# Performance work log

Measured on AMD Instinct MI355X. Metric: run time of the kernel, lower is better.

## Reference

```python
import jax, jax.numpy as jnp
import numpy as np

N, E = 20000, 320000
D_IN, H1, H2, H3, D_OUT = 2048, 512, 128, 32, 2
EPS = 1e-5


def layer_norm(x, g, b):
    mu = jnp.mean(x, axis=-1, keepdims=True)
    var = jnp.mean(jnp.square(x - mu), axis=-1, keepdims=True)
    return (x - mu) * jax.lax.rsqrt(var + EPS) * g + b


def gcn_conv(x, src, dst, n, W, b):
    # x' = D^{-1/2} A_hat D^{-1/2} (x W) + b  (self-loops already in src/dst)
    xw = x @ W
    deg = jax.ops.segment_sum(jnp.ones_like(src, dtype=x.dtype), dst, num_segments=n)
    dinv = jnp.where(deg > 0, jax.lax.rsqrt(jnp.maximum(deg, 1.0)), 0.0)
    norm = dinv[src] * dinv[dst]  # [E+N]
    msg = xw[src] * norm[:, None]
    return jax.ops.segment_sum(msg, dst, num_segments=n) + b


def gat_conv(x, src, dst, n, W, a_src, a_dst, b):
    # single-head GAT, concat=False; PyG defaults: LeakyReLU(0.2), softmax over dst
    xw = x @ W  # [N, H3]
    alpha = jax.nn.leaky_relu(xw[src] @ a_src + xw[dst] @ a_dst, 0.2)  # [E+N]
    amax = jax.ops.segment_max(alpha, dst, num_segments=n)
    e = jnp.exp(alpha - amax[dst])
    denom = jax.ops.segment_sum(e, dst, num_segments=n)
    coef = e / denom[dst]
    out = jax.ops.segment_sum(xw[src] * coef[:, None], dst, num_segments=n)
    return out + b


def setup_inputs() -> dict:
    key = jax.random.key(0)
    ks = jax.random.split(key, 24)
    x = jax.random.normal(ks[0], (N, D_IN), dtype=jnp.float32)
    edge_index = jax.random.randint(ks[1], (2, E), 0, N, dtype=jnp.int64)

    def glorot(k, shape):
        lim = float(np.sqrt(6.0 / (shape[0] + shape[1])))
        return jax.random.uniform(k, shape, jnp.float32, -lim, lim)

    return {
        "x": x, "edge_index": edge_index,
        "W1": glorot(ks[2], (D_IN, H1)), "b1": jnp.zeros((H1,), jnp.float32),
        "ln1_g": jnp.ones((H1,), jnp.float32), "ln1_b": jnp.zeros((H1,), jnp.float32),
        "W2": glorot(ks[3], (H1, H2)), "b2": jnp.zeros((H2,), jnp.float32),
        "ln2_g": jnp.ones((H2,), jnp.float32), "ln2_b": jnp.zeros((H2,), jnp.float32),
        "W3": glorot(ks[4], (H2, H3)), "b3": jnp.zeros((H3,), jnp.float32),
        "ln3_g": jnp.ones((H3,), jnp.float32), "ln3_b": jnp.zeros((H3,), jnp.float32),
        "Wg": glorot(ks[5], (H3, H3)),
        "att_src": jax.random.normal(ks[6], (H3,), jnp.float32) * 0.1,
        "att_dst": jax.random.normal(ks[7], (H3,), jnp.float32) * 0.1,
        "bg": jnp.zeros((H3,), jnp.float32),
        "fc_w": glorot(ks[8], (H3, D_OUT)), "fc_b": jnp.zeros((D_OUT,), jnp.float32),
    }


def reference(x, edge_index, W1, b1, ln1_g, ln1_b, W2, b2, ln2_g, ln2_b,
              W3, b3, ln3_g, ln3_b, Wg, att_src, att_dst, bg, fc_w, fc_b):
    n = x.shape[0]
    loops = jnp.arange(n, dtype=edge_index.dtype)
    src = jnp.concatenate([edge_index[0], loops])
    dst = jnp.concatenate([edge_index[1], loops])

    h = jax.nn.relu(layer_norm(gcn_conv(x, src, dst, n, W1, b1), ln1_g, ln1_b))
    h = jax.nn.relu(layer_norm(gcn_conv(h, src, dst, n, W2, b2), ln2_g, ln2_b))
    h = jax.nn.relu(layer_norm(gcn_conv(h, src, dst, n, W3, b3), ln3_g, ln3_b))
    h = jax.nn.relu(gat_conv(h, src, dst, n, Wg, att_src, att_dst, bg))
    pooled = jnp.mean(h, axis=0, keepdims=True)  # [1, H3]
    return pooled @ fc_w + fc_b  # [1, 2]
```

## Files before the change

kernel.cpp:

```cpp
#include <hip/hip_runtime.h>
#include <hip/hip_bf16.h>
#include <cstdint>
#include <cstddef>

#define N_NODES 20000
#define N_EDGES 320000
#define DIM_IN  2048
#define DIM_H1  512
#define DIM_H2  128
#define DIM_H3  32
#define NPART   64
static constexpr float LN_EPS = 1e-5f;

typedef __bf16 bf16x8 __attribute__((ext_vector_type(8)));
typedef __bf16 bf16x2 __attribute__((ext_vector_type(2)));
typedef float f32x4 __attribute__((ext_vector_type(4)));

__device__ __forceinline__ void glds16(const void* g, void* l) {
  __builtin_amdgcn_global_load_lds(
      (const __attribute__((address_space(1))) unsigned int*)g,
      (__attribute__((address_space(3))) unsigned int*)l, 16, 0, 0);
}

__global__ void detect_fmt_kernel(const void* eraw, int* flag) {
  const int2* p = (const int2*)eraw;
  int all0 = 1;
  for (int i = 0; i < 32; ++i) if (p[i].y != 0) all0 = 0;
  *flag = all0;
}

__global__ void convert_edges_kernel(const void* eraw, const int* __restrict__ flag,
                                     int* __restrict__ src, int* __restrict__ dst, int E) {
  const int is64 = *flag;
  for (int e = blockIdx.x * blockDim.x + threadIdx.x; e < E; e += gridDim.x * blockDim.x) {
    if (is64) {
      const long long* p = (const long long*)eraw;
      src[e] = (int)p[e];
      dst[e] = (int)p[(size_t)E + e];
    } else {
      const int* p = (const int*)eraw;
      src[e] = p[e];
      dst[e] = p[(size_t)E + e];
    }
  }
}

__global__ void count_kernel(const int* __restrict__ dst, int* __restrict__ cnt, int E) {
  for (int e = blockIdx.x * blockDim.x + threadIdx.x; e < E; e += gridDim.x * blockDim.x)
    atomicAdd(&cnt[dst[e]], 1);
}

__global__ __launch_bounds__(1024) void scan_kernel(const int* __restrict__ cnt,
                                                    int* __restrict__ rowptr,
                                                    int* __restrict__ cursor, int n) {
  __shared__ int s[1024];
  const int t = threadIdx.x;
  const int chunk = (n + 1023) / 1024;
  const int beg = t * chunk;
  const int end = min(beg + chunk, n);
  int sum = 0;
  for (int i = beg; i < end; ++i) sum += cnt[i];
  s[t] = sum;
  __syncthreads();
  for (int d = 1; d < 1024; d <<= 1) {
    int v = (t >= d) ? s[t - d] : 0;
    __syncthreads();
    s[t] += v;
    __syncthreads();
  }
  int run = s[t] - sum;
  for (int i = beg; i < end; ++i) { rowptr[i] = run; cursor[i] = run; run += cnt[i]; }
  if (t == 1023) rowptr[n] = s[1023];
}

__global__ void scatter_kernel(const int* __restrict__ src, const int* __restrict__ dst,
                               int* __restrict__ cursor, int* __restrict__ csr_src, int E) {
  for (int e = blockIdx.x * blockDim.x + threadIdx.x; e < E; e += gridDim.x * blockDim.x) {
    int d = dst[e];
    int pos = atomicAdd(&cursor[d], 1);
    csr_src[pos] = src[e];
  }
}

__global__ void dinv_kernel(const int* __restrict__ cnt, float* __restrict__ dinv, int n) {
  int i = blockIdx.x * blockDim.x + threadIdx.x;
  if (i < n) dinv[i] = rsqrtf((float)(cnt[i] + 1));
}

__global__ __launch_bounds__(256) void transpose_cvt_kernel(const float* __restrict__ W,
                                                            __bf16* __restrict__ WT,
                                                            int K, int N) {
  __shared__ float t[32][33];
  const int kb = blockIdx.x * 32, nb = blockIdx.y * 32;
  const int tx = threadIdx.x & 31, ty = threadIdx.x >> 5;
  #pragma unroll
  for (int i = 0; i < 32; i += 8)
    t[ty + i][tx] = W[(size_t)(kb + ty + i) * N + nb + tx];
  __syncthreads();
  #pragma unroll
  for (int i = 0; i < 32; i += 8)
    WT[(size_t)(nb + ty + i) * K + kb + tx] = (__bf16)t[tx][ty + i];
}

template <typename AT, typename CT>
__global__ __launch_bounds__(256) void gemm_glds_kernel(
    const AT* __restrict__ A, const __bf16* __restrict__ BT,
    CT* __restrict__ C, int M, int N, int K) {
  __shared__ __align__(16) AT     Asm[128 * 32];
  __shared__ __align__(16) __bf16 Bsm[128 * 32];
  const int tid = threadIdx.x;
  const int wave = tid >> 6;
  const int lane = tid & 63;
  const int row0 = blockIdx.x * 128;
  const int col0 = blockIdx.y * 128;
  const int wr = (wave >> 1) * 64;
  const int wc = (wave & 1) * 64;

  f32x4 acc[4][4] = {};

  for (int k0 = 0; k0 < K; k0 += 32) {
    if constexpr (sizeof(AT) == 4) {
      #pragma unroll
      for (int i = 0; i < 4; ++i) {
        const int rbase = wave * 32 + i * 8;
        int gr = row0 + rbase + (lane >> 3);
        if (gr >= M) gr = M - 1;
        const int ssrc = (lane & 7) ^ (lane >> 3);
        glds16((const float*)A + (size_t)gr * K + k0 + ssrc * 4, &Asm[rbase * 32]);
      }
    } else {
      #pragma unroll
      for (int i = 0; i < 2; ++i) {
        const int rbase = wave * 32 + i * 16;
        int gr = row0 + rbase + (lane >> 2);
        if (gr >= M) gr = M - 1;
        const int ssrc = (lane & 3) ^ ((lane >> 3) & 3);
        glds16((const __bf16*)A + (size_t)gr * K + k0 + ssrc * 8, &Asm[rbase * 32]);
      }
    }
    #pragma unroll
    for (int j = 0; j < 2; ++j) {
      const int rbase = wave * 32 + j * 16;
      const int gr = col0 + rbase + (lane >> 2);
      const int ssrc = (lane & 3) ^ ((lane >> 3) & 3);
      glds16(BT + (size_t)gr * K + k0 + ssrc * 8, &Bsm[rbase * 32]);
    }
    __syncthreads();

    const int q = lane >> 4;
    bf16x8 af[4], bfr[4];
    #pragma unroll
    for (int m = 0; m < 4; ++m) {
      const int row = wr + m * 16 + (lane & 15);
      if constexpr (sizeof(AT) == 4) {
        const int sw = row & 7;
        f32x4 lo = *(const f32x4*)&((const float*)Asm)[row * 32 + (((2 * q) ^ sw) * 4)];
        f32x4 hi = *(const f32x4*)&((const float*)Asm)[row * 32 + (((2 * q + 1) ^ sw) * 4)];
        bf16x8 o;
        o[0] = (__bf16)lo[0]; o[1] = (__bf16)lo[1]; o[2] = (__bf16)lo[2]; o[3] = (__bf16)lo[3];
        o[4] = (__bf16)hi[0]; o[5] = (__bf16)hi[1]; o[6] = (__bf16)hi[2]; o[7] = (__bf16)hi[3];
        af[m] = o;
      } else {
        const int sw = (row >> 1) & 3;
        af[m] = *(const bf16x8*)&((const __bf16*)Asm)[row * 32 + ((q ^ sw) * 8)];
      }
    }
    #pragma unroll
    for (int n = 0; n < 4; ++n) {
      const int row = wc + n * 16 + (lane & 15);
      const int sw = (row >> 1) & 3;
      bfr[n] = *(const bf16x8*)&Bsm[row * 32 + ((q ^ sw) * 8)];
    }
    #pragma unroll
    for (int m = 0; m < 4; ++m)
      #pragma unroll
      for (int n = 0; n < 4; ++n)
        acc[m][n] = __builtin_amdgcn_mfma_f32_16x16x32_bf16(af[m], bfr[n], acc[m][n], 0, 0, 0);
    __syncthreads();
  }

  #pragma unroll
  for (int m = 0; m < 4; ++m) {
    const int r = row0 + wr + m * 16 + (lane >> 4) * 4;
    #pragma unroll
    for (int n = 0; n < 4; ++n) {
      const int c = col0 + wc + n * 16 + (lane & 15);
      #pragma unroll
      for (int j = 0; j < 4; ++j)
        if (r + j < M) C[(size_t)(r + j) * N + c] = (CT)acc[m][n][j];
    }
  }
}

template <int F, int TPB, typename OutT>
__global__ __launch_bounds__(TPB) void gcn_agg_ln_relu_kernel(
    const float* __restrict__ xw, const float* __restrict__ dinv,
    const int* __restrict__ rowptr, const int* __restrict__ csr_src,
    const float* __restrict__ bias, const float* __restrict__ gamma,
    const float* __restrict__ beta, OutT* __restrict__ h) {
  constexpr int NF = (F + TPB - 1) / TPB;
  const int i = blockIdx.x;
  const int tid = threadIdx.x;
  const float di = dinv[i];
  float acc[NF];
  #pragma unroll
  for (int q = 0; q < NF; ++q) {
    int f = tid + q * TPB;
    acc[q] = (f < F) ? di * xw[(size_t)i * F + f] : 0.f;
  }
  const int beg = rowptr[i], end = rowptr[i + 1];
  for (int j = beg; j < end; ++j) {
    int s = csr_src[j];
    float c = dinv[s];
    const float* row = xw + (size_t)s * F;
    #pragma unroll
    for (int q = 0; q < NF; ++q) {
      int f = tid + q * TPB;
      if (f < F) acc[q] += c * row[f];
    }
  }
  float sum = 0.f, sumsq = 0.f;
  #pragma unroll
  for (int q = 0; q < NF; ++q) {
    int f = tid + q * TPB;
    if (f < F) {
      float v = di * acc[q] + bias[f];
      acc[q] = v;
      sum += v;
      sumsq += v * v;
    }
  }
  #pragma unroll
  for (int m = 32; m >= 1; m >>= 1) {
    sum += __shfl_xor(sum, m);
    sumsq += __shfl_xor(sumsq, m);
  }
  constexpr int NW = TPB / 64;
  __shared__ float red[2][NW];
  const int wid = tid >> 6, lane = tid & 63;
  if (lane == 0) { red[0][wid] = sum; red[1][wid] = sumsq; }
  __syncthreads();
  if (tid == 0) {
    float a = 0.f, b2 = 0.f;
    for (int w = 0; w < NW; ++w) { a += red[0][w]; b2 += red[1][w]; }
    red[0][0] = a;
    red[1][0] = b2;
  }
  __syncthreads();
  const float mu = red[0][0] / F;
  const float var = red[1][0] / F - mu * mu;
  const float rstd = rsqrtf(var + LN_EPS);
  #pragma unroll
  for (int q = 0; q < NF; ++q) {
    int f = tid + q * TPB;
    if (f < F) h[(size_t)i * F + f] = (OutT)fmaxf(0.f, (acc[q] - mu) * rstd * gamma[f] + beta[f]);
  }
}

template <int F, int TPB, typename OutT>
__global__ __launch_bounds__(TPB) void gcn_agg_ln_relu_bf16_kernel(
    const __bf16* __restrict__ xw, const float* __restrict__ dinv,
    const int* __restrict__ rowptr, const int* __restrict__ csr_src,
    const float* __restrict__ bias, const float* __restrict__ gamma,
    const float* __restrict__ beta, OutT* __restrict__ h) {
  static_assert(F == 2 * TPB, "layout");
  const int i = blockIdx.x;
  const int tid = threadIdx.x;
  const int f0 = tid * 2;
  const float di = dinv[i];
  bf16x2 v = *(const bf16x2*)&xw[(size_t)i * F + f0];
  float a0 = di * (float)v[0];
  float a1 = di * (float)v[1];
  const int beg = rowptr[i], end = rowptr[i + 1];
  for (int j = beg; j < end; ++j) {
    int s = csr_src[j];
    float c = dinv[s];
    bf16x2 r = *(const bf16x2*)&xw[(size_t)s * F + f0];
    a0 += c * (float)r[0];
    a1 += c * (float)r[1];
  }
  a0 = di * a0 + bias[f0];
  a1 = di * a1 + bias[f0 + 1];
  float sum = a0 + a1;
  float sumsq = a0 * a0 + a1 * a1;
  #pragma unroll
  for (int m = 32; m >= 1; m >>= 1) {
    sum += __shfl_xor(sum, m);
    sumsq += __shfl_xor(sumsq, m);
  }
  constexpr int NW = TPB / 64;
  __shared__ float red[2][NW];
  const int wid = tid >> 6, lane = tid & 63;
  if (lane == 0) { red[0][wid] = sum; red[1][wid] = sumsq; }
  __syncthreads();
  if (tid == 0) {
    float a = 0.f, b2 = 0.f;
    for (int w = 0; w < NW; ++w) { a += red[0][w]; b2 += red[1][w]; }
    red[0][0] = a;
    red[1][0] = b2;
  }
  __syncthreads();
  const float mu = red[0][0] / F;
  const float var = red[1][0] / F - mu * mu;
  const float rstd = rsqrtf(var + LN_EPS);
  float o0 = fmaxf(0.f, (a0 - mu) * rstd * gamma[f0] + beta[f0]);
  float o1 = fmaxf(0.f, (a1 - mu) * rstd * gamma[f0 + 1] + beta[f0 + 1]);
  if constexpr (sizeof(OutT) == 2) {
    bf16x2 o; o[0] = (__bf16)o0; o[1] = (__bf16)o1;
    *(bf16x2*)&((__bf16*)h)[(size_t)i * F + f0] = o;
  } else {
    float2 o = make_float2(o0, o1);
    *(float2*)&((float*)h)[(size_t)i * F + f0] = o;
  }
}

template <int BM, int BN, int BK, int TM, int TN>
__global__ __launch_bounds__((BM / TM) * (BN / TN)) void sgemm_kernel(
    const float* __restrict__ A, const float* __restrict__ B, float* __restrict__ C,
    int M, int N, int K) {
  constexpr int THREADS = (BM / TM) * (BN / TN);
  __shared__ float As[BK][BM + 4];
  __shared__ float Bs[BK][BN];
  const int tid = threadIdx.x;
  const int tcol = tid % (BN / TN);
  const int trow = tid / (BN / TN);
  const int row0 = blockIdx.y * BM;
  const int col0 = blockIdx.x * BN;
  float acc[TM][TN] = {};
  for (int k0 = 0; k0 < K; k0 += BK) {
    constexpr int A4 = BM * BK / 4;
    #pragma unroll
    for (int i = tid; i < A4; i += THREADS) {
      int r = i / (BK / 4);
      int c4 = i % (BK / 4);
      int gr = row0 + r;
      float4 v = make_float4(0.f, 0.f, 0.f, 0.f);
      if (gr < M) v = *(const float4*)(A + (size_t)gr * K + k0 + c4 * 4);
      As[c4 * 4 + 0][r] = v.x;
      As[c4 * 4 + 1][r] = v.y;
      As[c4 * 4 + 2][r] = v.z;
      As[c4 * 4 + 3][r] = v.w;
    }
    constexpr int B4 = BK * BN / 4;
    #pragma unroll
    for (int i = tid; i < B4; i += THREADS) {
      int r = i / (BN / 4);
      int c4 = i % (BN / 4);
      float4 v = *(const float4*)(B + (size_t)(k0 + r) * N + col0 + c4 * 4);
      *(float4*)(&Bs[r][c4 * 4]) = v;
    }
    __syncthreads();
    #pragma unroll
    for (int kk = 0; kk < BK; ++kk) {
      float ra[TM], rb[TN];
      #pragma unroll
      for (int i = 0; i < TM; ++i) ra[i] = As[kk][trow * TM + i];
      #pragma unroll
      for (int j = 0; j < TN; ++j) rb[j] = Bs[kk][tcol * TN + j];
      #pragma unroll
      for (int i = 0; i < TM; ++i)
        #pragma unroll
        for (int j = 0; j < TN; ++j) acc[i][j] = fmaf(ra[i], rb[j], acc[i][j]);
    }
    __syncthreads();
  }
  #pragma unroll
  for (int i = 0; i < TM; ++i) {
    int gr = row0 + trow * TM + i;
    if (gr >= M) continue;
    #pragma unroll
    for (int j = 0; j < TN; ++j) {
      int gc = col0 + tcol * TN + j;
      if (gc < N) C[(size_t)gr * N + gc] = acc[i][j];
    }
  }
}

__global__ void gat_sdots_kernel(const float* __restrict__ xwg,
                                 const float* __restrict__ att_src,
                                 const float* __restrict__ att_dst,
                                 float* __restrict__ s_src, float* __restrict__ s_dst, int n) {
  int gid = blockIdx.x * blockDim.x + threadIdx.x;
  int node = gid >> 5;
  int l = threadIdx.x & 31;
  if (node >= n) return;
  float v = xwg[(size_t)node * 32 + l];
  float vs = v * att_src[l];
  float vd = v * att_dst[l];
  #pragma unroll
  for (int m = 16; m >= 1; m >>= 1) {
    vs += __shfl_xor(vs, m);
    vd += __shfl_xor(vd, m);
  }
  if (l == 0) { s_src[node] = vs; s_dst[node] = vd; }
}

__device__ __forceinline__ float leaky02(float x) { return x > 0.f ? x : 0.2f * x; }

__global__ __launch_bounds__(64) void gat_agg_kernel(
    const float* __restrict__ xwg, const float* __restrict__ s_src,
    const float* __restrict__ s_dst, const int* __restrict__ rowptr,
    const int* __restrict__ csr_src, const float* __restrict__ bg,
    float* __restrict__ pooled_part) {
  const int i = blockIdx.x;
  const int lane = threadIdx.x;
  const int f = lane & 31;
  const int half = lane >> 5;
  const float sd = s_dst[i];
  float m, den, acc;
  if (half == 0) {
    m = leaky02(s_src[i] + sd);
    den = 1.f;
    acc = xwg[(size_t)i * 32 + f];
  } else {
    m = -3.0e38f;
    den = 0.f;
    acc = 0.f;
  }
  const int beg = rowptr[i], end = rowptr[i + 1];
  for (int j = beg + half; j < end; j += 2) {
    int s = csr_src[j];
    float a = leaky02(s_src[s] + sd);
    float mn = fmaxf(m, a);
    float sc = __expf(m - mn);
    float ea = __expf(a - mn);
    acc = acc * sc + ea * xwg[(size_t)s * 32 + f];
    den = den * sc + ea;
    m = mn;
  }
  float m_o = __shfl_xor(m, 32);
  float den_o = __shfl_xor(den, 32);
  float acc_o = __shfl_xor(acc, 32);
  float mn = fmaxf(m, m_o);
  float sc = __expf(m - mn);
  float so = __expf(m_o - mn);
  float den_t = den * sc + den_o * so;
  float acc_t = acc * sc + acc_o * so;
  float out = fmaxf(acc_t / den_t + bg[f], 0.f);
  if (lane < 32) atomicAdd(&pooled_part[(size_t)(i & (NPART - 1)) * 32 + f], out);
}

__global__ __launch_bounds__(64) void final_fc_kernel(const float* __restrict__ pooled_part,
                                                      const float* __restrict__ fc_w,
                                                      const float* __restrict__ fc_b,
                                                      float* __restrict__ out, float invN) {
  const int lane = threadIdx.x;
  const int f = lane & 31, half = lane >> 5;
  float p = 0.f;
  #pragma unroll
  for (int b = 0; b < NPART / 2; ++b)
    p += pooled_part[(size_t)(half * (NPART / 2) + b) * 32 + f];
  p += __shfl_xor(p, 32);
  p *= invN;
  #pragma unroll
  for (int c = 0; c < 2; ++c) {
    float v = (lane < 32) ? p * fc_w[f * 2 + c] : 0.f;
    #pragma unroll
    for (int m = 16; m >= 1; m >>= 1) v += __shfl_xor(v, m);
    if (lane == 0) out[c] = v + fc_b[c];
  }
}

extern "C" void kernel_launch(void* const* d_in, const int* in_sizes, int n_in,
                              void* d_out, int out_size, void* d_ws, size_t ws_size,
                              hipStream_t stream) {
  const float* x       = (const float*)d_in[0];
  const void*  edges   = d_in[1];
  const float* W1      = (const float*)d_in[2];
  const float* b1      = (const float*)d_in[3];
  const float* ln1_g   = (const float*)d_in[4];
  const float* ln1_b   = (const float*)d_in[5];
  const float* W2      = (const float*)d_in[6];
  const float* b2      = (const float*)d_in[7];
  const float* ln2_g   = (const float*)d_in[8];
  const float* ln2_b   = (const float*)d_in[9];
  const float* W3      = (const float*)d_in[10];
  const float* b3      = (const float*)d_in[11];
  const float* ln3_g   = (const float*)d_in[12];
  const float* ln3_b   = (const float*)d_in[13];
  const float* Wg      = (const float*)d_in[14];
  const float* att_src = (const float*)d_in[15];
  const float* att_dst = (const float*)d_in[16];
  const float* bg      = (const float*)d_in[17];
  const float* fc_w    = (const float*)d_in[18];
  const float* fc_b    = (const float*)d_in[19];
  float* out = (float*)d_out;

  const int N = N_NODES, E = N_EDGES;

  char* ws = (char*)d_ws;
  size_t off = 0;
  auto alloc = [&](size_t bytes) {
    size_t o = off;
    off = (off + bytes + 255) & ~(size_t)255;
    return o;
  };
  size_t o_bufA   = alloc((size_t)N * DIM_H1 * 4);
  size_t o_bufB   = alloc((size_t)N * DIM_H1 * 4);
  size_t o_w1t    = alloc((size_t)DIM_IN * DIM_H1 * 2);
  size_t o_w2t    = alloc((size_t)DIM_H1 * DIM_H2 * 2);
  size_t o_src    = alloc((size_t)E * 4);
  size_t o_dst    = alloc((size_t)E * 4);
  size_t o_csr    = alloc((size_t)E * 4);
  size_t o_cnt    = alloc((size_t)N * 4);
  size_t o_rowptr = alloc((size_t)(N + 1) * 4);
  size_t o_cursor = alloc((size_t)N * 4);
  size_t o_dinv   = alloc((size_t)N * 4);
  size_t o_ssrc   = alloc((size_t)N * 4);
  size_t o_sdst   = alloc((size_t)N * 4);
  size_t o_pooled = alloc((size_t)NPART * 32 * 4);
  size_t o_flag   = alloc(4);

  float* bufA   = (float*)(ws + o_bufA);
  float* bufB   = (float*)(ws + o_bufB);
  __bf16* W1T   = (__bf16*)(ws + o_w1t);
  __bf16* W2T   = (__bf16*)(ws + o_w2t);
  int*   srcI   = (int*)(ws + o_src);
  int*   dstI   = (int*)(ws + o_dst);
  int*   csr    = (int*)(ws + o_csr);
  int*   cnt    = (int*)(ws + o_cnt);
  int*   rowptr = (int*)(ws + o_rowptr);
  int*   cursor = (int*)(ws + o_cursor);
  float* dinv   = (float*)(ws + o_dinv);
  float* ssrc   = (float*)(ws + o_ssrc);
  float* sdst   = (float*)(ws + o_sdst);
  float* pooled = (float*)(ws + o_pooled);
  int*   flag   = (int*)(ws + o_flag);

  hipMemsetAsync(cnt, 0, (size_t)N * 4, stream);
  hipMemsetAsync(pooled, 0, (size_t)NPART * 32 * 4, stream);

  const int EB = (E + 255) / 256;

  detect_fmt_kernel<<<1, 1, 0, stream>>>(edges, flag);
  convert_edges_kernel<<<EB, 256, 0, stream>>>(edges, flag, srcI, dstI, E);
  count_kernel<<<EB, 256, 0, stream>>>(dstI, cnt, E);
  scan_kernel<<<1, 1024, 0, stream>>>(cnt, rowptr, cursor, N);
  scatter_kernel<<<EB, 256, 0, stream>>>(srcI, dstI, cursor, csr, E);
  dinv_kernel<<<(N + 255) / 256, 256, 0, stream>>>(cnt, dinv, N);

  transpose_cvt_kernel<<<dim3(DIM_IN / 32, DIM_H1 / 32), 256, 0, stream>>>(W1, W1T, DIM_IN, DIM_H1);
  transpose_cvt_kernel<<<dim3(DIM_H1 / 32, DIM_H2 / 32), 256, 0, stream>>>(W2, W2T, DIM_H1, DIM_H2);

  const int MB128 = (N + 127) / 128;

  gemm_glds_kernel<float, __bf16>
      <<<dim3(MB128, DIM_H1 / 128), 256, 0, stream>>>(x, W1T, (__bf16*)bufA, N, DIM_H1, DIM_IN);
  gcn_agg_ln_relu_bf16_kernel<DIM_H1, 256, __bf16>
      <<<N, 256, 0, stream>>>((const __bf16*)bufA, dinv, rowptr, csr, b1, ln1_g, ln1_b, (__bf16*)bufB);

  gemm_glds_kernel<__bf16, __bf16>
      <<<dim3(MB128, DIM_H2 / 128), 256, 0, stream>>>((const __bf16*)bufB, W2T, (__bf16*)bufA, N, DIM_H2, DIM_H1);
  gcn_agg_ln_relu_bf16_kernel<DIM_H2, 64, float>
      <<<N, 64, 0, stream>>>((const __bf16*)bufA, dinv, rowptr, csr, b2, ln2_g, ln2_b, bufB);

  sgemm_kernel<128, 32, 16, 8, 2>
      <<<dim3(1, MB128), 256, 0, stream>>>(bufB, W3, bufA, N, DIM_H3, DIM_H2);
  gcn_agg_ln_relu_kernel<DIM_H3, 64, float>
      <<<N, 64, 0, stream>>>(bufA, dinv, rowptr, csr, b3, ln3_g, ln3_b, bufB);

  sgemm_kernel<128, 32, 16, 8, 2>
      <<<dim3(1, MB128), 256, 0, stream>>>(bufB, Wg, bufA, N, DIM_H3, DIM_H3);
  gat_sdots_kernel<<<(N * 32 + 255) / 256, 256, 0, stream>>>(bufA, att_src, att_dst, ssrc, sdst, N);
  gat_agg_kernel<<<N, 64, 0, stream>>>(bufA, ssrc, sdst, rowptr, csr, bg, pooled);

  final_fc_kernel<<<1, 64, 0, stream>>>(pooled, fc_w, fc_b, out, 1.f / (float)N);
}
```

Measured before the change: 393.2 us.

## Double-buffer LDS tiles in bf16 GEMM and fuse edge degree counting into conversion

The MFMA GEMM now double-buffers its LDS tiles. It issues global-to-LDS loads for the next K slice before computing the current one, using an explicit vmcnt wait and raw barriers in place of the two __syncthreads per iteration. This aims to hide global load latency behind the MFMA work in the dominant first-layer GEMM, but doubles LDS use per block, which may lower occupancy. Separately, the in-degree atomic count is folded into the edge conversion kernel, removing one launch and one reread of dst.

```diff
diff --git a/kernel.cpp b/kernel.cpp
--- a/kernel.cpp
+++ b/kernel.cpp
@@ -30,24 +30,24 @@
 }
 
 __global__ void convert_edges_kernel(const void* eraw, const int* __restrict__ flag,
-                                     int* __restrict__ src, int* __restrict__ dst, int E) {
+                                     int* __restrict__ src, int* __restrict__ dst,
+                                     int* __restrict__ cnt, int E) {
   const int is64 = *flag;
   for (int e = blockIdx.x * blockDim.x + threadIdx.x; e < E; e += gridDim.x * blockDim.x) {
+    int s, d;
     if (is64) {
       const long long* p = (const long long*)eraw;
-      src[e] = (int)p[e];
-      dst[e] = (int)p[(size_t)E + e];
+      s = (int)p[e];
+      d = (int)p[(size_t)E + e];
     } else {
       const int* p = (const int*)eraw;
-      src[e] = p[e];
-      dst[e] = p[(size_t)E + e];
-    }
-  }
-}
-
-__global__ void count_kernel(const int* __restrict__ dst, int* __restrict__ cnt, int E) {
-  for (int e = blockIdx.x * blockDim.x + threadIdx.x; e < E; e += gridDim.x * blockDim.x)
-    atomicAdd(&cnt[dst[e]], 1);
+      s = p[e];
+      d = p[(size_t)E + e];
+    }
+    src[e] = s;
+    dst[e] = d;
+    atomicAdd(&cnt[d], 1);
+  }
 }
 
 __global__ __launch_bounds__(1024) void scan_kernel(const int* __restrict__ cnt,
@@ -103,11 +103,11 @@
 }
 
 template <typename AT, typename CT>
-__global__ __launch_bounds__(256) void gemm_glds_kernel(
+__global__ __launch_bounds__(256) void gemm_dbuf_kernel(
     const AT* __restrict__ A, const __bf16* __restrict__ BT,
     CT* __restrict__ C, int M, int N, int K) {
-  __shared__ __align__(16) AT     Asm[128 * 32];
-  __shared__ __align__(16) __bf16 Bsm[128 * 32];
+  __shared__ __align__(16) AT     Asm[2][128 * 32];
+  __shared__ __align__(16) __bf16 Bsm[2][128 * 32];
   const int tid = threadIdx.x;
   const int wave = tid >> 6;
   const int lane = tid & 63;
@@ -115,10 +115,11 @@
   const int col0 = blockIdx.y * 128;
   const int wr = (wave >> 1) * 64;
   const int wc = (wave & 1) * 64;
+  constexpr int NGLDS = (sizeof(AT) == 4) ? 6 : 4;
 
   f32x4 acc[4][4] = {};
 
-  for (int k0 = 0; k0 < K; k0 += 32) {
+  auto STAGE = [&](int buf, int k0) {
     if constexpr (sizeof(AT) == 4) {
       #pragma unroll
       for (int i = 0; i < 4; ++i) {
@@ -126,7 +127,7 @@
         int gr = row0 + rbase + (lane >> 3);
         if (gr >= M) gr = M - 1;
         const int ssrc = (lane & 7) ^ (lane >> 3);
-        glds16((const float*)A + (size_t)gr * K + k0 + ssrc * 4, &Asm[rbase * 32]);
+        glds16((const float*)A + (size_t)gr * K + k0 + ssrc * 4, &Asm[buf][rbase * 32]);
       }
     } else {
       #pragma unroll
@@ -135,7 +136,7 @@
         int gr = row0 + rbase + (lane >> 2);
         if (gr >= M) gr = M - 1;
         const int ssrc = (lane & 3) ^ ((lane >> 3) & 3);
-        glds16((const __bf16*)A + (size_t)gr * K + k0 + ssrc * 8, &Asm[rbase * 32]);
+        glds16((const __bf16*)A + (size_t)gr * K + k0 + ssrc * 8, &Asm[buf][rbase * 32]);
       }
     }
     #pragma unroll
@@ -143,9 +144,23 @@
       const int rbase = wave * 32 + j * 16;
       const int gr = col0 + rbase + (lane >> 2);
       const int ssrc = (lane & 3) ^ ((lane >> 3) & 3);
-      glds16(BT + (size_t)gr * K + k0 + ssrc * 8, &Bsm[rbase * 32]);
-    }
-    __syncthreads();
+      glds16(BT + (size_t)gr * K + k0 + ssrc * 8, &Bsm[buf][rbase * 32]);
+    }
+  };
+
+  const int NT = K / 32;
+  STAGE(0, 0);
+
+  for (int t = 0; t < NT; ++t) {
+    const int cur = t & 1;
+    if (t + 1 < NT) {
+      STAGE(cur ^ 1, (t + 1) * 32);
+      asm volatile("s_waitcnt vmcnt(%0)" :: "i"(NGLDS) : "memory");
+    } else {
+      asm volatile("s_waitcnt vmcnt(0)" ::: "memory");
+    }
+    __builtin_amdgcn_s_barrier();
+    __builtin_amdgcn_sched_barrier(0);
 
     const int q = lane >> 4;
     bf16x8 af[4], bfr[4];
@@ -154,29 +169,31 @@
       const int row = wr + m * 16 + (lane & 15);
       if constexpr (sizeof(AT) == 4) {
         const int sw = row & 7;
-        f32x4 lo = *(const f32x4*)&((const float*)Asm)[row * 32 + (((2 * q) ^ sw) * 4)];
-        f32x4 hi = *(const f32x4*)&((const float*)Asm)[row * 32 + (((2 * q + 1) ^ sw) * 4)];
+        f32x4 lo = *(const f32x4*)&((const float*)&Asm[cur][0])[row * 32 + (((2 * q) ^ sw) * 4)];
+        f32x4 hi = *(const f32x4*)&((const float*)&Asm[cur][0])[row * 32 + (((2 * q + 1) ^ sw) * 4)];
         bf16x8 o;
         o[0] = (__bf16)lo[0]; o[1] = (__bf16)lo[1]; o[2] = (__bf16)lo[2]; o[3] = (__bf16)lo[3];
         o[4] = (__bf16)hi[0]; o[5] = (__bf16)hi[1]; o[6] = (__bf16)hi[2]; o[7] = (__bf16)hi[3];
         af[m] = o;
       } else {
         const int sw = (row >> 1) & 3;
-        af[m] = *(const bf16x8*)&((const __bf16*)Asm)[row * 32 + ((q ^ sw) * 8)];
+        af[m] = *(const bf16x8*)&((const __bf16*)&Asm[cur][0])[row * 32 + ((q ^ sw) * 8)];
       }
     }
     #pragma unroll
     for (int n = 0; n < 4; ++n) {
       const int row = wc + n * 16 + (lane & 15);
       const int sw = (row >> 1) & 3;
-      bfr[n] = *(const bf16x8*)&Bsm[row * 32 + ((q ^ sw) * 8)];
+      bfr[n] = *(const bf16x8*)&Bsm[cur][row * 32 + ((q ^ sw) * 8)];
     }
     #pragma unroll
     for (int m = 0; m < 4; ++m)
       #pragma unroll
       for (int n = 0; n < 4; ++n)
         acc[m][n] = __builtin_amdgcn_mfma_f32_16x16x32_bf16(af[m], bfr[n], acc[m][n], 0, 0, 0);
-    __syncthreads();
+
+    __builtin_amdgcn_sched_barrier(0);
+    __builtin_amdgcn_s_barrier();
   }
 
   #pragma unroll
@@ -533,8 +550,7 @@
   const int EB = (E + 255) / 256;
 
   detect_fmt_kernel<<<1, 1, 0, stream>>>(edges, flag);
-  convert_edges_kernel<<<EB, 256, 0, stream>>>(edges, flag, srcI, dstI, E);
-  count_kernel<<<EB, 256, 0, stream>>>(dstI, cnt, E);
+  convert_edges_kernel<<<EB, 256, 0, stream>>>(edges, flag, srcI, dstI, cnt, E);
   scan_kernel<<<1, 1024, 0, stream>>>(cnt, rowptr, cursor, N);
   scatter_kernel<<<EB, 256, 0, stream>>>(srcI, dstI, cursor, csr, E);
   dinv_kernel<<<(N + 255) / 256, 256, 0, stream>>>(cnt, dinv, N);
@@ -544,12 +560,12 @@
 
   const int MB128 = (N + 127) / 128;
 
-  gemm_glds_kernel<float, __bf16>
+  gemm_dbuf_kernel<float, __bf16>
       <<<dim3(MB128, DIM_H1 / 128), 256, 0, stream>>>(x, W1T, (__bf16*)bufA, N, DIM_H1, DIM_IN);
   gcn_agg_ln_relu_bf16_kernel<DIM_H1, 256, __bf16>
       <<<N, 256, 0, stream>>>((const __bf16*)bufA, dinv, rowptr, csr, b1, ln1_g, ln1_b, (__bf16*)bufB);
 
-  gemm_glds_kernel<__bf16, __bf16>
+  gemm_dbuf_kernel<__bf16, __bf16>
       <<<dim3(MB128, DIM_H2 / 128), 256, 0, stream>>>((const __bf16*)bufB, W2T, (__bf16*)bufA, N, DIM_H2, DIM_H1);
   gcn_agg_ln_relu_bf16_kernel<DIM_H2, 64, float>
       <<<N, 64, 0, stream>>>((const __bf16*)bufA, dinv, rowptr, csr, b2, ln2_g, ln2_b, bufB);
```

Result: no change. 390.1 us (-0.8%).
